# Optimization experiments

Hardware: AMD Instinct MI355X
Metric: run time of the kernel (lower is better)

The kernel has to match this reference:

```python
import jax, jax.numpy as jnp
from jax import lax
import numpy as np

B, N, G, K = 4, 1024, 128, 32
D_MODEL, DEPTH, CLS = 384, 12, 40
D_INNER, D_STATE, D_CONV, DT_RANK = 768, 16, 4, 24
EPS = 1e-5
BN_SCALE = 1.0 / float(np.sqrt(1.0 + EPS))  # eval BN, running_mean=0, running_var=1


def layernorm(x, w, b):
    mu = x.mean(-1, keepdims=True)
    var = ((x - mu) ** 2).mean(-1, keepdims=True)
    return (x - mu) * lax.rsqrt(var + EPS) * w + b


def bn_eval(x, g, b):
    return x * (g * BN_SCALE) + b


def fps(xyz, n):
    Bb, Nn, _ = xyz.shape
    first = jnp.zeros((Bb,), jnp.int32)

    def step(carry, _):
        dmin, last = carry
        p = jnp.take_along_axis(xyz, last[:, None, None], axis=1)  # B,1,3
        dmin = jnp.minimum(dmin, jnp.sum((xyz - p) ** 2, -1))
        nxt = jnp.argmax(dmin, -1).astype(jnp.int32)
        return (dmin, nxt), nxt

    _, rest = lax.scan(step, (jnp.full((Bb, Nn), 1e10, xyz.dtype), first), None, length=n - 1)
    return jnp.concatenate([first[None, :], rest], 0).T  # B,G


def group_points(xyz):
    idx = fps(xyz, G)
    center = jnp.take_along_axis(xyz, idx[:, :, None], axis=1)            # B,G,3
    d2 = jnp.sum((center[:, :, None, :] - xyz[:, None, :, :]) ** 2, -1)   # B,G,N
    _, knn = lax.top_k(-d2, K)                                            # B,G,K
    nb = jax.vmap(lambda p, i: p[i])(xyz, knn)                            # B,G,K,3
    return nb - center[:, :, None, :], center


def encoder(pg, w1, b1, g1, bb1, w2, b2, w3, b3, g2, bb2, w4, b4):
    Bb, Gg, Kk, _ = pg.shape
    f = pg.reshape(Bb * Gg, Kk, 3)
    f = jax.nn.relu(bn_eval(f @ w1.T + b1, g1, bb1))                      # BG,K,128
    f = f @ w2.T + b2                                                     # BG,K,256
    fg = f.max(1, keepdims=True)
    f = jnp.concatenate([jnp.broadcast_to(fg, f.shape), f], -1)           # BG,K,512
    f = jax.nn.relu(bn_eval(f @ w3.T + b3, g2, bb2))
    f = f @ w4.T + b4
    return f.max(1).reshape(Bb, Gg, -1)                                   # B,G,C


def mamba_mixer(x, ipw, cw, cb, xpw, dpw, dpb, A_log, Dp, opw):
    L = x.shape[1]
    xz = x @ ipw.T                                                        # B,L,2*Di
    u, z = jnp.split(xz, 2, -1)
    up = jnp.pad(u, ((0, 0), (D_CONV - 1, 0), (0, 0)))                    # causal depthwise conv
    u = sum(up[:, k:k + L, :] * cw[:, k] for k in range(D_CONV)) + cb
    u = jax.nn.silu(u)
    xdb = u @ xpw.T
    dt, Bm, Cm = jnp.split(xdb, [DT_RANK, DT_RANK + D_STATE], -1)
    dt = jax.nn.softplus(dt @ dpw.T + dpb)                                # B,L,Di
    A = -jnp.exp(A_log)                                                   # Di,Ds

    def step(h, inp):
        dt_t, B_t, C_t, u_t = inp
        h = jnp.exp(dt_t[:, :, None] * A) * h + (dt_t * u_t)[:, :, None] * B_t[:, None, :]
        return h, jnp.einsum('bds,bs->bd', h, C_t)

    h0 = jnp.zeros((x.shape[0], D_INNER, D_STATE), x.dtype)
    _, ys = lax.scan(step, h0, (dt.swapaxes(0, 1), Bm.swapaxes(0, 1), Cm.swapaxes(0, 1), u.swapaxes(0, 1)))
    y = ys.swapaxes(0, 1) + u * Dp
    return (y * jax.nn.silu(z)) @ opw.T


def forward(pts, enc_w1, enc_b1, enc_bn1_g, enc_bn1_b, enc_w2, enc_b2, enc_w3, enc_b3,
            enc_bn2_g, enc_bn2_b, enc_w4, enc_b4, pos_w1, pos_b1, pos_w2, pos_b2,
            ln_w, ln_b, in_proj_w, conv_w, conv_b, x_proj_w, dt_proj_w, dt_proj_b,
            A_log, D_param, out_proj_w, normf_w, normf_b, norm_w, norm_b,
            head_w1, head_b1, head_bn1_g, head_bn1_b, head_w2, head_b2,
            head_bn2_g, head_bn2_b, head_w3, head_b3):
    nb, center = group_points(pts)
    tok = encoder(nb, enc_w1, enc_b1, enc_bn1_g, enc_bn1_b, enc_w2, enc_b2,
                  enc_w3, enc_b3, enc_bn2_g, enc_bn2_b, enc_w4, enc_b4)    # B,G,384
    pos = jax.nn.gelu(center @ pos_w1.T + pos_b1, approximate=False) @ pos_w2.T + pos_b2

    # PointMamba token reordering: sort by center x, y, z and concatenate -> L = 3G
    toks, poss = [], []
    for ax in range(3):
        o = jnp.argsort(center[:, :, ax], axis=-1)[:, :, None]
        toks.append(jnp.take_along_axis(tok, o, axis=1))
        poss.append(jnp.take_along_axis(pos, o, axis=1))
    tok = jnp.concatenate(toks, 1)
    pos = jnp.concatenate(poss, 1)

    h = tok + pos
    res = jnp.zeros_like(h)

    def layer_step(carry, p):
        h, res = carry
        lnw, lnb, ipw, cw, cb, xpw, dpw, dpb, Al, Dp, opw = p
        res = h + res
        x = layernorm(res, lnw, lnb)
        h = mamba_mixer(x, ipw, cw, cb, xpw, dpw, dpb, Al, Dp, opw)
        return (h, res), None

    (h, res), _ = lax.scan(layer_step, (h, res),
                           (ln_w, ln_b, in_proj_w, conv_w, conv_b, x_proj_w,
                            dt_proj_w, dt_proj_b, A_log, D_param, out_proj_w))
    x = layernorm(h + res, normf_w, normf_b)   # MixerModel.norm_f
    x = layernorm(x, norm_w, norm_b)           # PointMamba.norm
    feat = x.mean(1)                           # B,384
    h1 = jax.nn.relu(bn_eval(feat @ head_w1.T + head_b1, head_bn1_g, head_bn1_b))
    h2 = jax.nn.relu(bn_eval(h1 @ head_w2.T + head_b2, head_bn2_g, head_bn2_b))
    return h2 @ head_w3.T + head_b3            # B,CLS


def setup_inputs():
    key = jax.random.key(0)
    ks = iter(jax.random.split(key, 64))

    def rn(shape, s=0.02):
        return jax.random.normal(next(ks), shape, jnp.float32) * s

    inp = dict(
        pts=jax.random.normal(next(ks), (B, N, 3), jnp.float32),
        enc_w1=rn((128, 3), 0.1), enc_b1=jnp.zeros((128,)),
        enc_bn1_g=jnp.ones((128,)), enc_bn1_b=jnp.zeros((128,)),
        enc_w2=rn((256, 128), 0.05), enc_b2=jnp.zeros((256,)),
        enc_w3=rn((512, 512), 0.05), enc_b3=jnp.zeros((512,)),
        enc_bn2_g=jnp.ones((512,)), enc_bn2_b=jnp.zeros((512,)),
        enc_w4=rn((D_MODEL, 512), 0.05), enc_b4=jnp.zeros((D_MODEL,)),
        pos_w1=rn((128, 3), 0.1), pos_b1=jnp.zeros((128,)),
        pos_w2=rn((D_MODEL, 128), 0.05), pos_b2=jnp.zeros((D_MODEL,)),
        ln_w=jnp.ones((DEPTH, D_MODEL)), ln_b=jnp.zeros((DEPTH, D_MODEL)),
        in_proj_w=rn((DEPTH, 2 * D_INNER, D_MODEL)),
        conv_w=rn((DEPTH, D_INNER, D_CONV), 0.2), conv_b=jnp.zeros((DEPTH, D_INNER)),
        x_proj_w=rn((DEPTH, DT_RANK + 2 * D_STATE, D_INNER)),
        dt_proj_w=rn((DEPTH, D_INNER, DT_RANK), 0.1),
        dt_proj_b=jnp.full((DEPTH, D_INNER), -4.6, jnp.float32),
        A_log=jnp.broadcast_to(jnp.log(jnp.arange(1, D_STATE + 1, dtype=jnp.float32)),
                               (DEPTH, D_INNER, D_STATE)).copy(),
        D_param=jnp.ones((DEPTH, D_INNER)),
        out_proj_w=rn((DEPTH, D_MODEL, D_INNER)),
        normf_w=jnp.ones((D_MODEL,)), normf_b=jnp.zeros((D_MODEL,)),
        norm_w=jnp.ones((D_MODEL,)), norm_b=jnp.zeros((D_MODEL,)),
        head_w1=rn((256, D_MODEL), 0.05), head_b1=jnp.zeros((256,)),
        head_bn1_g=jnp.ones((256,)), head_bn1_b=jnp.zeros((256,)),
        head_w2=rn((256, 256), 0.05), head_b2=jnp.zeros((256,)),
        head_bn2_g=jnp.ones((256,)), head_bn2_b=jnp.zeros((256,)),
        head_w3=rn((CLS, 256), 0.05), head_b3=jnp.zeros((CLS,)),
    )
    return inp


def reference(pts, enc_w1, enc_b1, enc_bn1_g, enc_bn1_b, enc_w2, enc_b2, enc_w3, enc_b3,
              enc_bn2_g, enc_bn2_b, enc_w4, enc_b4, pos_w1, pos_b1, pos_w2, pos_b2,
              ln_w, ln_b, in_proj_w, conv_w, conv_b, x_proj_w, dt_proj_w, dt_proj_b,
              A_log, D_param, out_proj_w, normf_w, normf_b, norm_w, norm_b,
              head_w1, head_b1, head_bn1_g, head_bn1_b, head_w2, head_b2,
              head_bn2_g, head_bn2_b, head_w3, head_b3):
    return forward(pts, enc_w1, enc_b1, enc_bn1_g, enc_bn1_b, enc_w2, enc_b2, enc_w3, enc_b3,
                   enc_bn2_g, enc_bn2_b, enc_w4, enc_b4, pos_w1, pos_b1, pos_w2, pos_b2,
                   ln_w, ln_b, in_proj_w, conv_w, conv_b, x_proj_w, dt_proj_w, dt_proj_b,
                   A_log, D_param, out_proj_w, normf_w, normf_b, norm_w, norm_b,
                   head_w1, head_b1, head_bn1_g, head_bn1_b, head_w2, head_b2,
                   head_bn2_g, head_bn2_b, head_w3, head_b3)
```

## Files before the change

kernel.cpp:

```cpp
#include <hip/hip_runtime.h>
#include <hip/hip_bf16.h>

using bf16 = __hip_bfloat16;
using short8  = __attribute__((ext_vector_type(8))) short;
using floatx4 = __attribute__((ext_vector_type(4))) float;
using ull = unsigned long long;

constexpr int Bn = 4, Np = 1024, Gn = 128, Kn = 32;
constexpr int DM = 384, DEPTH = 12, CLSn = 40;
constexpr int DI = 768, DSt = 16, DTR = 24;
constexpr int Ln = 384;
constexpr int NCH = 12, CHS = 32;
constexpr int NLC = 24;
constexpr float EPSf = 1e-5f;
constexpr float BNS = 0.99999500003749968752f;
constexpr float LOG2E = 1.4426950408889634f;

static __device__ __forceinline__ short f2bf(float f){
  bf16 h = __float2bfloat16(f);
  return *reinterpret_cast<short*>(&h);
}
static __device__ __forceinline__ float fsig(float x){ return 1.f/(1.f + __expf(-x)); }
static __device__ __forceinline__ float fsoftplus(float x){
  return fmaxf(x, 0.f) + __logf(1.f + __expf(-fabsf(x)));
}

template<int CTRL>
static __device__ __forceinline__ int dppmov(int x){
  return __builtin_amdgcn_update_dpp(0, x, CTRL, 0xF, 0xF, true);
}
static __device__ __forceinline__ ull redmax64(ull key){
  #define RSTEP(CTRL) { \
    int hi = (int)(unsigned)(key >> 32), lo = (int)(unsigned)key; \
    int h2 = dppmov<CTRL>(hi), l2 = dppmov<CTRL>(lo); \
    ull k2 = ((ull)(unsigned)h2 << 32) | (unsigned)l2; \
    if (k2 > key) key = k2; }
  RSTEP(0x111) RSTEP(0x112) RSTEP(0x114) RSTEP(0x118) RSTEP(0x142) RSTEP(0x143)
  #undef RSTEP
  return key;
}

__global__ __launch_bounds__(64) void fps_kernel(const float* __restrict__ pts,
                                                 float* __restrict__ center){
  int b = blockIdx.x, t = threadIdx.x;
  __shared__ float xs[1024], ys[1024], zs[1024];
  const float* p = pts + (size_t)b * Np * 3;
  float D[16];
  #pragma unroll
  for (int i = 0; i < 16; ++i){
    int n = t + 64*i;
    xs[n] = p[n*3+0]; ys[n] = p[n*3+1]; zs[n] = p[n*3+2];
    D[i] = 1e10f;
  }
  float px = xs[0], py = ys[0], pz = zs[0];
  if (t == 0){
    center[(size_t)(b*Gn)*3+0] = px;
    center[(size_t)(b*Gn)*3+1] = py;
    center[(size_t)(b*Gn)*3+2] = pz;
  }
  for (int it = 1; it < Gn; ++it){
    float v = -1.f; int nbest = t;
    #pragma unroll
    for (int i = 0; i < 16; ++i){
      int n = t + 64*i;
      float dx = __fsub_rn(xs[n], px);
      float dy = __fsub_rn(ys[n], py);
      float dz = __fsub_rn(zs[n], pz);
      float d  = __fadd_rn(__fadd_rn(__fmul_rn(dx,dx), __fmul_rn(dy,dy)), __fmul_rn(dz,dz));
      float dm = fminf(D[i], d); D[i] = dm;
      if (dm > v){ v = dm; nbest = n; }
    }
    ull key = ((ull)__float_as_uint(v) << 32) | (unsigned)(Np-1 - nbest);
    key = redmax64(key);
    int lo63 = __builtin_amdgcn_readlane((int)(unsigned)(key & 0xFFFFFFFFu), 63);
    int wn = Np-1 - lo63;
    wn = min(max(wn, 0), Np-1);
    px = xs[wn]; py = ys[wn]; pz = zs[wn];
    if (t == 0){
      center[(size_t)(b*Gn+it)*3+0] = px;
      center[(size_t)(b*Gn+it)*3+1] = py;
      center[(size_t)(b*Gn+it)*3+2] = pz;
    }
  }
}

__global__ __launch_bounds__(256) void knn_kernel(const float* __restrict__ pts,
                                                  const float* __restrict__ center,
                                                  float* __restrict__ nb){
  int gid = blockIdx.x; int b = gid >> 7;
  __shared__ float d2[1024];
  __shared__ float rv[4]; __shared__ int ri[4];
  int t = threadIdx.x;
  float cx = center[(size_t)gid*3+0], cy = center[(size_t)gid*3+1], cz = center[(size_t)gid*3+2];
  const float* p = pts + (size_t)b * Np * 3;
  for (int n = t; n < Np; n += 256){
    float dx = __fsub_rn(cx, p[n*3+0]);
    float dy = __fsub_rn(cy, p[n*3+1]);
    float dz = __fsub_rn(cz, p[n*3+2]);
    d2[n] = __fadd_rn(__fadd_rn(__fmul_rn(dx,dx), __fmul_rn(dy,dy)), __fmul_rn(dz,dz));
  }
  __syncthreads();
  for (int kk = 0; kk < Kn; ++kk){
    float v = 3e38f; int idx = 0;
    for (int n = t; n < Np; n += 256){
      float d = d2[n];
      if (d < v || (d == v && n < idx)){ v = d; idx = n; }
    }
    ull key = ((ull)(unsigned)(~__float_as_uint(v)) << 32) | (unsigned)(Np-1 - idx);
    key = redmax64(key);
    if ((t & 63) == 63){
      rv[t>>6] = __uint_as_float(~(unsigned)(key >> 32));
      ri[t>>6] = Np-1 - (int)(unsigned)(key & 0xFFFFFFFFu);
    }
    __syncthreads();
    if (t == 0){
      float bv = rv[0]; int bi = ri[0];
      for (int w = 1; w < 4; ++w){
        if (rv[w] < bv || (rv[w] == bv && ri[w] < bi)){ bv = rv[w]; bi = ri[w]; }
      }
      bi = min(max(bi, 0), Np-1);
      nb[((size_t)gid*Kn+kk)*3+0] = __fsub_rn(p[bi*3+0], cx);
      nb[((size_t)gid*Kn+kk)*3+1] = __fsub_rn(p[bi*3+1], cy);
      nb[((size_t)gid*Kn+kk)*3+2] = __fsub_rn(p[bi*3+2], cz);
      d2[bi] = 3e38f;
    }
    __syncthreads();
  }
}

__global__ __launch_bounds__(256) void cvt_bf16(const float* __restrict__ s,
                                                bf16* __restrict__ d, int n){
  int i = (blockIdx.x*256 + threadIdx.x)*4;
  if (i < n){
    float4 v = *(const float4*)(s + i);
    short* o = (short*)d + i;
    o[0] = f2bf(v.x); o[1] = f2bf(v.y); o[2] = f2bf(v.z); o[3] = f2bf(v.w);
  }
}

template<typename AT, typename WT, int ACT, int GATE>
__global__ __launch_bounds__(256) void gemm_mfma(const AT* __restrict__ A, int lda,
                                                 const WT* __restrict__ W,
                                                 const float* __restrict__ bias,
                                                 const float* __restrict__ g,
                                                 const float* __restrict__ bb,
                                                 float* __restrict__ C, int ldc,
                                                 int M, int N, int K){
  __shared__ __align__(16) short As[64*40];
  __shared__ __align__(16) short Ws[64*40];
  int bm = blockIdx.x * 64, bn = blockIdx.y * 64;
  int t = threadIdx.x;
  int row = t >> 2;
  int kseg = (t & 3) * 8;
  int w = t >> 6, lane = t & 63, m16 = lane & 15, q = lane >> 4;
  bool kvec = ((K & 3) == 0) && ((lda & 3) == 0 || sizeof(AT) == 2);
  floatx4 acc[4] = {};
  for (int k0 = 0; k0 < K; k0 += 32){
    if constexpr (GATE){
      const float* Ar = (const float*)A + (size_t)(bm + row)*lda + k0 + kseg;
      float4 y0 = *(const float4*)Ar;
      float4 y1 = *(const float4*)(Ar + 4);
      float4 z0 = *(const float4*)(Ar + 768);
      float4 z1 = *(const float4*)(Ar + 772);
      short* dst = &As[row*40 + kseg];
      dst[0] = f2bf(y0.x * (z0.x * fsig(z0.x)));
      dst[1] = f2bf(y0.y * (z0.y * fsig(z0.y)));
      dst[2] = f2bf(y0.z * (z0.z * fsig(z0.z)));
      dst[3] = f2bf(y0.w * (z0.w * fsig(z0.w)));
      dst[4] = f2bf(y1.x * (z1.x * fsig(z1.x)));
      dst[5] = f2bf(y1.y * (z1.y * fsig(z1.y)));
      dst[6] = f2bf(y1.z * (z1.z * fsig(z1.z)));
      dst[7] = f2bf(y1.w * (z1.w * fsig(z1.w)));
    } else if constexpr (sizeof(AT) == 2){
      *(short8*)&As[row*40 + kseg] =
          *(const short8*)((const short*)A + (size_t)(bm + row)*lda + k0 + kseg);
    } else {
      const float* Ar = (const float*)A + (size_t)(bm + row)*lda;
      short* dst = &As[row*40 + kseg];
      if (kvec && (k0 + kseg + 8 <= K)){
        float4 a0 = *(const float4*)(Ar + k0 + kseg);
        float4 a1 = *(const float4*)(Ar + k0 + kseg + 4);
        dst[0]=f2bf(a0.x); dst[1]=f2bf(a0.y); dst[2]=f2bf(a0.z); dst[3]=f2bf(a0.w);
        dst[4]=f2bf(a1.x); dst[5]=f2bf(a1.y); dst[6]=f2bf(a1.z); dst[7]=f2bf(a1.w);
      } else {
        #pragma unroll
        for (int j = 0; j < 8; ++j){
          int k = k0 + kseg + j;
          dst[j] = (k < K) ? f2bf(Ar[k]) : (short)0;
        }
      }
    }
    if constexpr (sizeof(WT) == 2){
      int n = bn + row;
      short8 v;
      #pragma unroll
      for (int j = 0; j < 8; ++j) v[j] = 0;
      if (n < N) v = *(const short8*)((const short*)W + (size_t)n*K + k0 + kseg);
      *(short8*)&Ws[row*40 + kseg] = v;
    } else {
      int n = bn + row;
      short* dst = &Ws[row*40 + kseg];
      if (n < N && ((K & 3) == 0) && (k0 + kseg + 8 <= K)){
        const float* Wr = (const float*)W + (size_t)n*K + k0 + kseg;
        float4 w0 = *(const float4*)Wr;
        float4 w1 = *(const float4*)(Wr + 4);
        dst[0]=f2bf(w0.x); dst[1]=f2bf(w0.y); dst[2]=f2bf(w0.z); dst[3]=f2bf(w0.w);
        dst[4]=f2bf(w1.x); dst[5]=f2bf(w1.y); dst[6]=f2bf(w1.z); dst[7]=f2bf(w1.w);
      } else {
        #pragma unroll
        for (int j = 0; j < 8; ++j){
          int k = k0 + kseg + j;
          dst[j] = (n < N && k < K) ? f2bf(((const float*)W)[(size_t)n*K + k]) : (short)0;
        }
      }
    }
    __syncthreads();
    short8 af = *(const short8*)&As[(w*16 + m16)*40 + q*8];
    #pragma unroll
    for (int j = 0; j < 4; ++j){
      short8 bfr = *(const short8*)&Ws[(j*16 + m16)*40 + q*8];
      acc[j] = __builtin_amdgcn_mfma_f32_16x16x32_bf16(af, bfr, acc[j], 0, 0, 0);
    }
    __syncthreads();
  }
  #pragma unroll
  for (int j = 0; j < 4; ++j){
    int n = bn + j*16 + m16;
    if (n < N){
      float bv = bias ? bias[n] : 0.f;
      float gv = 0.f, bbv = 0.f;
      if (ACT == 1){ gv = g[n] * BNS; bbv = bb[n]; }
      #pragma unroll
      for (int r = 0; r < 4; ++r){
        int m = bm + w*16 + q*4 + r;
        float v = acc[j][r] + bv;
        if (ACT == 1){ v = v * gv + bbv; v = fmaxf(v, 0.f); }
        C[(size_t)m*ldc + n] = v;
      }
    }
  }
}

__global__ __launch_bounds__(256) void maxk_fg(float* __restrict__ f3in){
  int gg = blockIdx.x; int c = threadIdx.x;
  float m = -3e38f;
  for (int k = 0; k < Kn; ++k) m = fmaxf(m, f3in[((size_t)gg*Kn + k)*512 + 256 + c]);
  for (int k = 0; k < Kn; ++k) f3in[((size_t)gg*Kn + k)*512 + c] = m;
}

__global__ __launch_bounds__(384) void maxk_tok(const float* __restrict__ f4, float* __restrict__ tok){
  int gg = blockIdx.x; int c = threadIdx.x;
  float m = -3e38f;
  for (int k = 0; k < Kn; ++k) m = fmaxf(m, f4[((size_t)gg*Kn + k)*DM + c]);
  tok[(size_t)gg*DM + c] = m;
}

__global__ __launch_bounds__(128) void pos_kernel(const float* __restrict__ center,
                                                  const float* __restrict__ w1, const float* __restrict__ b1,
                                                  const float* __restrict__ w2, const float* __restrict__ b2,
                                                  float* __restrict__ tok){
  int gid = blockIdx.x;
  __shared__ float h1[128]; __shared__ float c3[3];
  int t = threadIdx.x;
  if (t < 3) c3[t] = center[(size_t)gid*3 + t];
  __syncthreads();
  float a = w1[t*3+0]*c3[0] + w1[t*3+1]*c3[1] + w1[t*3+2]*c3[2] + b1[t];
  h1[t] = 0.5f * a * (1.f + erff(a * 0.70710678118654752440f));
  __syncthreads();
  for (int c = t; c < DM; c += 128){
    float s = b2[c];
    for (int j = 0; j < 128; ++j) s += w2[(size_t)c*128 + j] * h1[j];
    tok[(size_t)gid*DM + c] += s;
  }
}

__global__ __launch_bounds__(128) void sort_kernel(const float* __restrict__ center,
                                                   int* __restrict__ order){
  int bax = blockIdx.x; int b = bax / 3, ax = bax % 3;
  __shared__ float key[128];
  int t = threadIdx.x;
  key[t] = center[(size_t)(b*Gn + t)*3 + ax];
  __syncthreads();
  float kt = key[t]; int r = 0;
  for (int j = 0; j < Gn; ++j){
    float kj = key[j];
    r += (kj < kt || (kj == kt && j < t)) ? 1 : 0;
  }
  r = min(max(r, 0), Gn-1);
  order[b*Ln + ax*Gn + r] = t;
}

__global__ __launch_bounds__(256) void build_h(const float* __restrict__ tok,
                        const int* __restrict__ order,
                        float* __restrict__ h, float* __restrict__ res){
  int i = blockIdx.x * blockDim.x + threadIdx.x;
  if (i >= Bn*Ln*DM) return;
  int c = i % DM; int l = (i / DM) % Ln; int b = i / (DM*Ln);
  int src = order[b*Ln + l];
  src = min(max(src, 0), Gn-1);
  h[i] = tok[((size_t)(b*Gn + src))*DM + c];
  res[i] = 0.f;
}

__global__ __launch_bounds__(256) void ln_res_kernel(const float* __restrict__ h,
                                                     float* __restrict__ res,
                                                     bf16* __restrict__ x,
                                                     const float* __restrict__ w,
                                                     const float* __restrict__ bias){
  int wv = threadIdx.x >> 6, ln = threadIdx.x & 63;
  int tokid = blockIdx.x*4 + wv;
  const float* hr = h + (size_t)tokid*DM;
  float* rr = res + (size_t)tokid*DM;
  bf16* xr = x + (size_t)tokid*DM;
  float v[6]; float s = 0.f;
  #pragma unroll
  for (int i = 0; i < 6; ++i){ int c = ln + 64*i; float t = hr[c] + rr[c]; rr[c] = t; v[i] = t; s += t; }
  #pragma unroll
  for (int o = 32; o > 0; o >>= 1) s += __shfl_xor(s, o);
  float mu = s * (1.f/DM);
  float q = 0.f;
  #pragma unroll
  for (int i = 0; i < 6; ++i){ float d = v[i] - mu; q += d*d; }
  #pragma unroll
  for (int o = 32; o > 0; o >>= 1) q += __shfl_xor(q, o);
  float rstd = rsqrtf(q * (1.f/DM) + EPSf);
  #pragma unroll
  for (int i = 0; i < 6; ++i){ int c = ln + 64*i;
    xr[c] = __float2bfloat16((v[i]-mu)*rstd*w[c] + bias[c]); }
}

__global__ __launch_bounds__(256) void conv_fused(const float* __restrict__ xz,
                                                  float* __restrict__ ucv,
                                                  const float* __restrict__ cw,
                                                  const float* __restrict__ cb){
  int blk = blockIdx.x;
  int lc = blk % NLC; int bd = blk / NLC; int dch = bd % 3; int b = bd / 3;
  int t = threadIdx.x; int d = dch*256 + t;
  int l0 = lc*16;
  float w0 = cw[d*4+0], w1 = cw[d*4+1], w2 = cw[d*4+2], w3 = cw[d*4+3];
  float bias = cb[d];
  float u0 = (l0 >= 3) ? xz[((size_t)(b*Ln + l0-3))*1536 + d] : 0.f;
  float u1 = (l0 >= 2) ? xz[((size_t)(b*Ln + l0-2))*1536 + d] : 0.f;
  float u2 = (l0 >= 1) ? xz[((size_t)(b*Ln + l0-1))*1536 + d] : 0.f;
  const float* pin = xz + ((size_t)(b*Ln + l0))*1536 + d;
  float* pout = ucv + ((size_t)(b*Ln + l0))*DI + d;
  float r[16];
  #pragma unroll
  for (int i = 0; i < 16; ++i) r[i] = pin[(size_t)i*1536];
  #pragma unroll
  for (int i = 0; i < 16; ++i){
    float v = u0*w0 + u1*w1 + u2*w2 + r[i]*w3 + bias;
    pout[(size_t)i*DI] = v * fsig(v);
    u0 = u1; u1 = u2; u2 = r[i];
  }
}

__global__ __launch_bounds__(256) void conv_save(const float* __restrict__ xz,
                                                 float* __restrict__ bnd){
  int blk = blockIdx.x;
  int lc = blk % NLC; int bd = blk / NLC; int dch = bd % 3; int b = bd / 3;
  int t = threadIdx.x; int d = dch*256 + t;
  int l0 = lc*16;
  #pragma unroll
  for (int j = 0; j < 3; ++j){
    int l = l0 - 3 + j;
    float v = (l >= 0) ? xz[((size_t)(b*Ln + l))*1536 + d] : 0.f;
    bnd[(((size_t)blk)*3 + j)*256 + t] = v;
  }
}

__global__ __launch_bounds__(256) void conv_apply(float* __restrict__ xz,
                                                  const float* __restrict__ bnd,
                                                  const float* __restrict__ cw,
                                                  const float* __restrict__ cb){
  int blk = blockIdx.x;
  int lc = blk % NLC; int bd = blk / NLC; int dch = bd % 3; int b = bd / 3;
  int t = threadIdx.x; int d = dch*256 + t;
  int l0 = lc*16;
  float w0 = cw[d*4+0], w1 = cw[d*4+1], w2 = cw[d*4+2], w3 = cw[d*4+3];
  float bias = cb[d];
  float u0 = bnd[(((size_t)blk)*3 + 0)*256 + t];
  float u1 = bnd[(((size_t)blk)*3 + 1)*256 + t];
  float u2 = bnd[(((size_t)blk)*3 + 2)*256 + t];
  float* p = xz + ((size_t)(b*Ln + l0))*1536 + d;
  float r[16];
  #pragma unroll
  for (int i = 0; i < 16; ++i) r[i] = p[(size_t)i*1536];
  #pragma unroll
  for (int i = 0; i < 16; ++i){
    float v = u0*w0 + u1*w1 + u2*w2 + r[i]*w3 + bias;
    p[(size_t)i*1536] = v * fsig(v);
    u0 = u1; u1 = u2; u2 = r[i];
  }
}

__global__ __launch_bounds__(256) void scanA_kernel(const float* __restrict__ usrc, int uld,
                                                    const float* __restrict__ xdb,
                                                    const float* __restrict__ dpw,
                                                    const float* __restrict__ dpb,
                                                    const float* __restrict__ A_log,
                                                    float* __restrict__ SB_S,
                                                    float* __restrict__ SB_dt){
  __shared__ float sRow[CHS*56];
  __shared__ float sU[CHS*256];
  int blk = blockIdx.x;
  int c = blk % NCH; int bd = blk / NCH; int dch = bd % 3; int b = bd / 3;
  int t = threadIdx.x; int d = dch*256 + t;
  int l0 = c*CHS;
  for (int i = t; i < CHS*56; i += 256) sRow[i] = xdb[((size_t)(b*Ln + l0))*56 + i];
  const float* up = usrc + ((size_t)(b*Ln + l0))*uld + dch*256;
  #pragma unroll
  for (int i = 0; i < CHS; ++i) sU[i*256 + t] = up[(size_t)i*uld + t];
  float w[DTR];
  const float* wp = dpw + (size_t)d*DTR;
  #pragma unroll
  for (int j = 0; j < DTR; ++j) w[j] = wp[j];
  float a2[DSt], h[DSt];
  const float* ap = A_log + (size_t)d*DSt;
  #pragma unroll
  for (int s = 0; s < DSt; ++s){ a2[s] = -__expf(ap[s]) * LOG2E; h[s] = 0.f; }
  float dbias = dpb[d];
  float sumdt = 0.f;
  __syncthreads();
  for (int i = 0; i < CHS; ++i){
    int ro = i*56;
    float dtr = dbias;
    #pragma unroll
    for (int j = 0; j < DTR; ++j) dtr += w[j] * sRow[ro + j];
    float dtv = fsoftplus(dtr);
    sumdt += dtv;
    float du = dtv * sU[i*256 + t];
    #pragma unroll
    for (int s = 0; s < DSt; ++s)
      h[s] = exp2f(dtv * a2[s]) * h[s] + du * sRow[ro + 24 + s];
  }
  size_t sb = ((size_t)blk*256 + t)*16;
  #pragma unroll
  for (int s = 0; s < DSt; ++s) SB_S[sb + s] = h[s];
  SB_dt[(size_t)blk*256 + t] = sumdt;
}

__global__ __launch_bounds__(256) void scanB_kernel(float* __restrict__ xz,
                                                    const float* __restrict__ usrc, int uld,
                                                    const float* __restrict__ xdb,
                                                    const float* __restrict__ dpw,
                                                    const float* __restrict__ dpb,
                                                    const float* __restrict__ A_log,
                                                    const float* __restrict__ Dp,
                                                    const float* __restrict__ SB_S,
                                                    const float* __restrict__ SB_dt){
  __shared__ float sRow[CHS*56];
  __shared__ float sU[CHS*256];
  int blk = blockIdx.x;
  int c = blk % NCH; int bd = blk / NCH; int dch = bd % 3; int b = bd / 3;
  int t = threadIdx.x; int d = dch*256 + t;
  int l0 = c*CHS;
  for (int i = t; i < CHS*56; i += 256) sRow[i] = xdb[((size_t)(b*Ln + l0))*56 + i];
  const float* up = usrc + ((size_t)(b*Ln + l0))*uld + dch*256;
  #pragma unroll
  for (int i = 0; i < CHS; ++i) sU[i*256 + t] = up[(size_t)i*uld + t];
  float w[DTR];
  const float* wp = dpw + (size_t)d*DTR;
  #pragma unroll
  for (int j = 0; j < DTR; ++j) w[j] = wp[j];
  float a2[DSt], h[DSt];
  const float* ap = A_log + (size_t)d*DSt;
  #pragma unroll
  for (int s = 0; s < DSt; ++s){ a2[s] = -__expf(ap[s]) * LOG2E; h[s] = 0.f; }
  for (int cc = 0; cc < c; ++cc){
    size_t base = (((size_t)bd*NCH + cc)*256 + t)*16;
    float sd = SB_dt[((size_t)bd*NCH + cc)*256 + t];
    #pragma unroll
    for (int s = 0; s < DSt; ++s)
      h[s] = exp2f(sd * a2[s]) * h[s] + SB_S[base + s];
  }
  float dbias = dpb[d];
  float Dd = Dp[d];
  float* ydst = xz + ((size_t)(b*Ln + l0))*1536 + dch*256;
  __syncthreads();
  for (int i = 0; i < CHS; ++i){
    int ro = i*56;
    float dtr = dbias;
    #pragma unroll
    for (int j = 0; j < DTR; ++j) dtr += w[j] * sRow[ro + j];
    float dtv = fsoftplus(dtr);
    float u = sU[i*256 + t];
    float du = dtv * u;
    float yv = 0.f;
    #pragma unroll
    for (int s = 0; s < DSt; ++s){
      h[s] = exp2f(dtv * a2[s]) * h[s] + du * sRow[ro + 24 + s];
      yv += h[s] * sRow[ro + 40 + s];
    }
    ydst[(size_t)i*1536 + t] = yv + u*Dd;
  }
}

__global__ __launch_bounds__(256) void final_ln_kernel(const float* __restrict__ h,
                                                       const float* __restrict__ res,
                                                       const float* w1, const float* b1,
                                                       const float* w2, const float* b2,
                                                       float* __restrict__ x){
  int wv = threadIdx.x >> 6, ln = threadIdx.x & 63;
  int tokid = blockIdx.x*4 + wv;
  const float* hr = h + (size_t)tokid*DM;
  const float* rr = res + (size_t)tokid*DM;
  float* xr = x + (size_t)tokid*DM;
  float v[6]; float s = 0.f;
  #pragma unroll
  for (int i = 0; i < 6; ++i){ int c = ln + 64*i; v[i] = hr[c] + rr[c]; s += v[i]; }
  #pragma unroll
  for (int o = 32; o > 0; o >>= 1) s += __shfl_xor(s, o);
  float mu = s * (1.f/DM); float q = 0.f;
  #pragma unroll
  for (int i = 0; i < 6; ++i){ float dd = v[i]-mu; q += dd*dd; }
  #pragma unroll
  for (int o = 32; o > 0; o >>= 1) q += __shfl_xor(q, o);
  float rstd = rsqrtf(q * (1.f/DM) + EPSf);
  float u[6]; float s2 = 0.f;
  #pragma unroll
  for (int i = 0; i < 6; ++i){ int c = ln + 64*i; u[i] = (v[i]-mu)*rstd*w1[c] + b1[c]; s2 += u[i]; }
  #pragma unroll
  for (int o = 32; o > 0; o >>= 1) s2 += __shfl_xor(s2, o);
  float mu2 = s2 * (1.f/DM); float q2 = 0.f;
  #pragma unroll
  for (int i = 0; i < 6; ++i){ float dd = u[i]-mu2; q2 += dd*dd; }
  #pragma unroll
  for (int o = 32; o > 0; o >>= 1) q2 += __shfl_xor(q2, o);
  float rstd2 = rsqrtf(q2 * (1.f/DM) + EPSf);
  #pragma unroll
  for (int i = 0; i < 6; ++i){ int c = ln + 64*i; xr[c] = (u[i]-mu2)*rstd2*w2[c] + b2[c]; }
}

__global__ __launch_bounds__(384) void head_kernel(const float* __restrict__ x,
    const float* w1, const float* b1, const float* g1, const float* bb1,
    const float* w2, const float* b2, const float* g2, const float* bb2,
    const float* w3, const float* b3, float* __restrict__ out){
  int b = blockIdx.x; int t = threadIdx.x;
  __shared__ float feat[DM]; __shared__ float h1[256]; __shared__ float h2[256];
  float s = 0.f;
  for (int l = 0; l < Ln; ++l) s += x[((size_t)(b*Ln + l))*DM + t];
  feat[t] = s * (1.f/Ln);
  __syncthreads();
  if (t < 256){
    float a = b1[t];
    for (int j = 0; j < DM; ++j) a += w1[(size_t)t*DM + j] * feat[j];
    a = a * (g1[t] * BNS) + bb1[t];
    h1[t] = fmaxf(a, 0.f);
  }
  __syncthreads();
  if (t < 256){
    float a = b2[t];
    for (int j = 0; j < 256; ++j) a += w2[(size_t)t*256 + j] * h1[j];
    a = a * (g2[t] * BNS) + bb2[t];
    h2[t] = fmaxf(a, 0.f);
  }
  __syncthreads();
  if (t < CLSn){
    float a = b3[t];
    for (int j = 0; j < 256; ++j) a += w3[(size_t)t*256 + j] * h2[j];
    out[b*CLSn + t] = a;
  }
}

extern "C" void kernel_launch(void* const* d_in, const int* in_sizes, int n_in,
                              void* d_out, int out_size, void* d_ws, size_t ws_size,
                              hipStream_t stream) {
  if (n_in < 42) return;
  if (out_size < Bn*CLSn) return;
  constexpr size_t WS_FLOATS = 3919936;
  if (ws_size < WS_FLOATS * sizeof(float)) return;
  constexpr size_t MIDF = 5812224;
  constexpr size_t BIGF = 18874368;
  const bool mid = ws_size >= (WS_FLOATS + MIDF) * sizeof(float);
  const bool big = ws_size >= (WS_FLOATS + MIDF + BIGF) * sizeof(float);

  const float* pts       = (const float*)d_in[0];
  const float* enc_w1    = (const float*)d_in[1];  const float* enc_b1    = (const float*)d_in[2];
  const float* enc_bn1_g = (const float*)d_in[3];  const float* enc_bn1_b = (const float*)d_in[4];
  const float* enc_w2    = (const float*)d_in[5];  const float* enc_b2    = (const float*)d_in[6];
  const float* enc_w3    = (const float*)d_in[7];  const float* enc_b3    = (const float*)d_in[8];
  const float* enc_bn2_g = (const float*)d_in[9];  const float* enc_bn2_b = (const float*)d_in[10];
  const float* enc_w4    = (const float*)d_in[11]; const float* enc_b4    = (const float*)d_in[12];
  const float* pos_w1    = (const float*)d_in[13]; const float* pos_b1    = (const float*)d_in[14];
  const float* pos_w2    = (const float*)d_in[15]; const float* pos_b2    = (const float*)d_in[16];
  const float* ln_w      = (const float*)d_in[17]; const float* ln_b      = (const float*)d_in[18];
  const float* in_proj_w = (const float*)d_in[19];
  const float* conv_w    = (const float*)d_in[20]; const float* conv_b    = (const float*)d_in[21];
  const float* x_proj_w  = (const float*)d_in[22];
  const float* dt_proj_w = (const float*)d_in[23]; const float* dt_proj_b = (const float*)d_in[24];
  const float* A_log     = (const float*)d_in[25]; const float* D_param   = (const float*)d_in[26];
  const float* out_proj_w= (const float*)d_in[27];
  const float* normf_w   = (const float*)d_in[28]; const float* normf_b   = (const float*)d_in[29];
  const float* norm_w    = (const float*)d_in[30]; const float* norm_b    = (const float*)d_in[31];
  const float* head_w1   = (const float*)d_in[32]; const float* head_b1   = (const float*)d_in[33];
  const float* head_bn1_g= (const float*)d_in[34]; const float* head_bn1_b= (const float*)d_in[35];
  const float* head_w2   = (const float*)d_in[36]; const float* head_b2   = (const float*)d_in[37];
  const float* head_bn2_g= (const float*)d_in[38]; const float* head_bn2_b= (const float*)d_in[39];
  const float* head_w3   = (const float*)d_in[40]; const float* head_b3   = (const float*)d_in[41];

  float* ws = (float*)d_ws;
  float* hb   = ws;
  float* resb = ws + 589824;
  float* U    = ws + 1179648;
  float* center = U;
  float* nb     = U + 1536;
  float* tok    = U + 50688;
  int*   order  = (int*)(U + 247296);
  float* eb0    = U + 262144;
  float* eb1    = U + 1310720;
  float* xz   = U;
  float* xdb  = U + 2359296;
  bf16*  xb   = (bf16*)(U + 2445312);
  float* SBdt = U + 2445312;
  float* BND  = U + 2482176;
  float* SBS  = hb;
  float* xf   = U;
  float* WB = ws + WS_FLOATS;
  bf16* wb_ip = (bf16*)WB;
  bf16* wb_op = (bf16*)(WB + 3538944);
  bf16* wb_xp = (bf16*)(WB + 5308416);
  bf16* wb_e2 = (bf16*)(WB + 5566464);
  bf16* wb_e3 = (bf16*)(WB + 5582848);
  bf16* wb_e4 = (bf16*)(WB + 5713920);
  float* F3in = WB + MIDF;
  float* F3   = WB + MIDF + 8388608;
  float* F1   = WB + MIDF + 16777216;
  float* F4   = F3in;
  float* ucv  = F3in;

  if (mid){
    cvt_bf16<<<(12*1536*384/4 + 255)/256, 256, 0, stream>>>(in_proj_w, wb_ip, 12*1536*384);
    cvt_bf16<<<(12*384*768/4 + 255)/256, 256, 0, stream>>>(out_proj_w, wb_op, 12*384*768);
    cvt_bf16<<<(12*56*768/4 + 255)/256, 256, 0, stream>>>(x_proj_w, wb_xp, 12*56*768);
    cvt_bf16<<<(256*128/4 + 255)/256, 256, 0, stream>>>(enc_w2, wb_e2, 256*128);
    cvt_bf16<<<(512*512/4 + 255)/256, 256, 0, stream>>>(enc_w3, wb_e3, 512*512);
    cvt_bf16<<<(384*512/4 + 255)/256, 256, 0, stream>>>(enc_w4, wb_e4, 384*512);
  }

  fps_kernel<<<Bn, 64, 0, stream>>>(pts, center);
  knn_kernel<<<Bn*Gn, 256, 0, stream>>>(pts, center, nb);

  if (big){
    gemm_mfma<float,float,1,0><<<dim3(256,2), 256, 0, stream>>>(nb, 3, enc_w1, enc_b1,
        enc_bn1_g, enc_bn1_b, F1, 128, 16384, 128, 3);
    gemm_mfma<float,bf16,0,0><<<dim3(256,4), 256, 0, stream>>>(F1, 128, wb_e2, enc_b2,
        nullptr, nullptr, F3in + 256, 512, 16384, 256, 128);
    maxk_fg<<<512, 256, 0, stream>>>(F3in);
    gemm_mfma<float,bf16,1,0><<<dim3(256,8), 256, 0, stream>>>(F3in, 512, wb_e3, enc_b3,
        enc_bn2_g, enc_bn2_b, F3, 512, 16384, 512, 512);
    gemm_mfma<float,bf16,0,0><<<dim3(256,6), 256, 0, stream>>>(F3, 512, wb_e4, enc_b4,
        nullptr, nullptr, F4, 384, 16384, 384, 512);
    maxk_tok<<<512, 384, 0, stream>>>(F4, tok);
  } else {
    for (int ch = 0; ch < 8; ++ch){
      const float* nb_c = nb + (size_t)ch*2048*3;
      float* tok_c = tok + (size_t)ch*64*DM;
      gemm_mfma<float,float,1,0><<<dim3(32,2), 256, 0, stream>>>(nb_c, 3, enc_w1, enc_b1,
          enc_bn1_g, enc_bn1_b, eb1, 128, 2048, 128, 3);
      if (mid){
        gemm_mfma<float,bf16,0,0><<<dim3(32,4), 256, 0, stream>>>(eb1, 128, wb_e2, enc_b2,
            nullptr, nullptr, eb0 + 256, 512, 2048, 256, 128);
        maxk_fg<<<64, 256, 0, stream>>>(eb0);
        gemm_mfma<float,bf16,1,0><<<dim3(32,8), 256, 0, stream>>>(eb0, 512, wb_e3, enc_b3,
            enc_bn2_g, enc_bn2_b, eb1, 512, 2048, 512, 512);
        gemm_mfma<float,bf16,0,0><<<dim3(32,6), 256, 0, stream>>>(eb1, 512, wb_e4, enc_b4,
            nullptr, nullptr, eb0, 384, 2048, 384, 512);
      } else {
        gemm_mfma<float,float,0,0><<<dim3(32,4), 256, 0, stream>>>(eb1, 128, enc_w2, enc_b2,
            nullptr, nullptr, eb0 + 256, 512, 2048, 256, 128);
        maxk_fg<<<64, 256, 0, stream>>>(eb0);
        gemm_mfma<float,float,1,0><<<dim3(32,8), 256, 0, stream>>>(eb0, 512, enc_w3, enc_b3,
            enc_bn2_g, enc_bn2_b, eb1, 512, 2048, 512, 512);
        gemm_mfma<float,float,0,0><<<dim3(32,6), 256, 0, stream>>>(eb1, 512, enc_w4, enc_b4,
            nullptr, nullptr, eb0, 384, 2048, 384, 512);
      }
      maxk_tok<<<64, 384, 0, stream>>>(eb0, tok_c);
    }
  }

  pos_kernel<<<Bn*Gn, 128, 0, stream>>>(center, pos_w1, pos_b1, pos_w2, pos_b2, tok);
  sort_kernel<<<Bn*3, 128, 0, stream>>>(center, order);
  build_h<<<(Bn*Ln*DM + 255)/256, 256, 0, stream>>>(tok, order, hb, resb);

  for (int l = 0; l < DEPTH; ++l){
    const float* lnw  = ln_w      + (size_t)l*DM;
    const float* lnb  = ln_b      + (size_t)l*DM;
    const float* ipw  = in_proj_w + (size_t)l*1536*DM;
    const float* cw   = conv_w    + (size_t)l*DI*4;
    const float* cb   = conv_b    + (size_t)l*DI;
    const float* xpw  = x_proj_w  + (size_t)l*56*DI;
    const float* dpw  = dt_proj_w + (size_t)l*DI*DTR;
    const float* dpb  = dt_proj_b + (size_t)l*DI;
    const float* Alg  = A_log     + (size_t)l*DI*DSt;
    const float* Dpar = D_param   + (size_t)l*DI;
    const float* opw  = out_proj_w+ (size_t)l*DM*DI;

    ln_res_kernel<<<Bn*Ln/4, 256, 0, stream>>>(hb, resb, xb, lnw, lnb);
    if (mid){
      gemm_mfma<bf16,bf16,0,0><<<dim3(24,24), 256, 0, stream>>>(xb, DM,
          wb_ip + (size_t)l*1536*DM, nullptr, nullptr, nullptr, xz, 1536, Bn*Ln, 1536, DM);
    } else {
      gemm_mfma<bf16,float,0,0><<<dim3(24,24), 256, 0, stream>>>(xb, DM, ipw,
          nullptr, nullptr, nullptr, xz, 1536, Bn*Ln, 1536, DM);
    }
    if (big){
      conv_fused<<<Bn*3*NLC, 256, 0, stream>>>(xz, ucv, cw, cb);
      if (mid)
        gemm_mfma<float,bf16,0,0><<<dim3(24,1), 256, 0, stream>>>(ucv, DI,
            wb_xp + (size_t)l*56*DI, nullptr, nullptr, nullptr, xdb, 56, Bn*Ln, 56, DI);
      else
        gemm_mfma<float,float,0,0><<<dim3(24,1), 256, 0, stream>>>(ucv, DI, xpw,
            nullptr, nullptr, nullptr, xdb, 56, Bn*Ln, 56, DI);
      scanA_kernel<<<Bn*3*NCH, 256, 0, stream>>>(ucv, DI, xdb, dpw, dpb, Alg, SBS, SBdt);
      scanB_kernel<<<Bn*3*NCH, 256, 0, stream>>>(xz, ucv, DI, xdb, dpw, dpb, Alg, Dpar, SBS, SBdt);
    } else {
      conv_save<<<Bn*3*NLC, 256, 0, stream>>>(xz, BND);
      conv_apply<<<Bn*3*NLC, 256, 0, stream>>>(xz, BND, cw, cb);
      if (mid)
        gemm_mfma<float,bf16,0,0><<<dim3(24,1), 256, 0, stream>>>(xz, 1536,
            wb_xp + (size_t)l*56*DI, nullptr, nullptr, nullptr, xdb, 56, Bn*Ln, 56, DI);
      else
        gemm_mfma<float,float,0,0><<<dim3(24,1), 256, 0, stream>>>(xz, 1536, xpw,
            nullptr, nullptr, nullptr, xdb, 56, Bn*Ln, 56, DI);
      scanA_kernel<<<Bn*3*NCH, 256, 0, stream>>>(xz, 1536, xdb, dpw, dpb, Alg, SBS, SBdt);
      scanB_kernel<<<Bn*3*NCH, 256, 0, stream>>>(xz, xz, 1536, xdb, dpw, dpb, Alg, Dpar, SBS, SBdt);
    }
    if (mid){
      gemm_mfma<float,bf16,0,1><<<dim3(24,6), 256, 0, stream>>>(xz, 1536,
          wb_op + (size_t)l*DM*DI, nullptr, nullptr, nullptr, hb, DM, Bn*Ln, DM, DI);
    } else {
      gemm_mfma<float,float,0,1><<<dim3(24,6), 256, 0, stream>>>(xz, 1536, opw,
          nullptr, nullptr, nullptr, hb, DM, Bn*Ln, DM, DI);
    }
  }

  final_ln_kernel<<<Bn*Ln/4, 256, 0, stream>>>(hb, resb, normf_w, normf_b, norm_w, norm_b, xf);
  head_kernel<<<Bn, 384, 0, stream>>>(xf, head_w1, head_b1, head_bn1_g, head_bn1_b,
                                      head_w2, head_b2, head_bn2_g, head_bn2_b,
                                      head_w3, head_b3, (float*)d_out);
}
```

Baseline: 1.786 ms.

## Fuse causal conv into x_proj GEMM and scan kernels, halve scan chunk size

Removes the separate conv_fused kernel on the big-workspace path. The depthwise causal conv plus SiLU is recomputed inside the x_proj GEMM's A-tile load and inside both scan kernels. The scan now writes y to a separate buffer with 16-row chunks, doubling the number of blocks. The gated out_proj GEMM reads y and z from different buffers. FPS keeps point coordinates in registers instead of re-reading LDS, and adds a missing sync; the trade-off is redundant conv arithmetic and extra xz reads, in exchange for fewer launches and a lost intermediate write.

New measurement: 2.074 ms. +16.2%, slower.

```diff
diff --git a/kernel.cpp b/kernel.cpp
--- a/kernel.cpp
+++ b/kernel.cpp
@@ -10,7 +10,6 @@
 constexpr int DM = 384, DEPTH = 12, CLSn = 40;
 constexpr int DI = 768, DSt = 16, DTR = 24;
 constexpr int Ln = 384;
-constexpr int NCH = 12, CHS = 32;
 constexpr int NLC = 24;
 constexpr float EPSf = 1e-5f;
 constexpr float BNS = 0.99999500003749968752f;
@@ -45,13 +44,16 @@
   int b = blockIdx.x, t = threadIdx.x;
   __shared__ float xs[1024], ys[1024], zs[1024];
   const float* p = pts + (size_t)b * Np * 3;
-  float D[16];
+  float X[16], Y[16], Z[16], D[16];
   #pragma unroll
   for (int i = 0; i < 16; ++i){
     int n = t + 64*i;
-    xs[n] = p[n*3+0]; ys[n] = p[n*3+1]; zs[n] = p[n*3+2];
+    float a = p[n*3+0], c = p[n*3+1], e = p[n*3+2];
+    X[i] = a; Y[i] = c; Z[i] = e;
+    xs[n] = a; ys[n] = c; zs[n] = e;
     D[i] = 1e10f;
   }
+  __syncthreads();
   float px = xs[0], py = ys[0], pz = zs[0];
   if (t == 0){
     center[(size_t)(b*Gn)*3+0] = px;
@@ -62,13 +64,12 @@
     float v = -1.f; int nbest = t;
     #pragma unroll
     for (int i = 0; i < 16; ++i){
-      int n = t + 64*i;
-      float dx = __fsub_rn(xs[n], px);
-      float dy = __fsub_rn(ys[n], py);
-      float dz = __fsub_rn(zs[n], pz);
+      float dx = __fsub_rn(X[i], px);
+      float dy = __fsub_rn(Y[i], py);
+      float dz = __fsub_rn(Z[i], pz);
       float d  = __fadd_rn(__fadd_rn(__fmul_rn(dx,dx), __fmul_rn(dy,dy)), __fmul_rn(dz,dz));
       float dm = fminf(D[i], d); D[i] = dm;
-      if (dm > v){ v = dm; nbest = n; }
+      if (dm > v){ v = dm; nbest = t + 64*i; }
     }
     ull key = ((ull)__float_as_uint(v) << 32) | (unsigned)(Np-1 - nbest);
     key = redmax64(key);
@@ -138,12 +139,12 @@
   }
 }
 
-template<typename AT, typename WT, int ACT, int GATE>
+template<typename AT, typename WT, int ACT, int MODE>
 __global__ __launch_bounds__(256) void gemm_mfma(const AT* __restrict__ A, int lda,
                                                  const WT* __restrict__ W,
                                                  const float* __restrict__ bias,
-                                                 const float* __restrict__ g,
-                                                 const float* __restrict__ bb,
+                                                 const float* __restrict__ gz,
+                                                 const float* __restrict__ bbp,
                                                  float* __restrict__ C, int ldc,
                                                  int M, int N, int K){
   __shared__ __align__(16) short As[64*40];
@@ -156,21 +157,36 @@
   bool kvec = ((K & 3) == 0) && ((lda & 3) == 0 || sizeof(AT) == 2);
   floatx4 acc[4] = {};
   for (int k0 = 0; k0 < K; k0 += 32){
-    if constexpr (GATE){
-      const float* Ar = (const float*)A + (size_t)(bm + row)*lda + k0 + kseg;
-      float4 y0 = *(const float4*)Ar;
-      float4 y1 = *(const float4*)(Ar + 4);
-      float4 z0 = *(const float4*)(Ar + 768);
-      float4 z1 = *(const float4*)(Ar + 772);
+    if constexpr (MODE == 1){
+      const float* Yr = (const float*)A + (size_t)(bm + row)*lda + k0 + kseg;
+      const float* Zr = gz + (size_t)(bm + row)*1536 + 768 + k0 + kseg;
+      float y[8], z[8];
+      *(float4*)&y[0] = *(const float4*)Yr;  *(float4*)&y[4] = *(const float4*)(Yr + 4);
+      *(float4*)&z[0] = *(const float4*)Zr;  *(float4*)&z[4] = *(const float4*)(Zr + 4);
       short* dst = &As[row*40 + kseg];
-      dst[0] = f2bf(y0.x * (z0.x * fsig(z0.x)));
-      dst[1] = f2bf(y0.y * (z0.y * fsig(z0.y)));
-      dst[2] = f2bf(y0.z * (z0.z * fsig(z0.z)));
-      dst[3] = f2bf(y0.w * (z0.w * fsig(z0.w)));
-      dst[4] = f2bf(y1.x * (z1.x * fsig(z1.x)));
-      dst[5] = f2bf(y1.y * (z1.y * fsig(z1.y)));
-      dst[6] = f2bf(y1.z * (z1.z * fsig(z1.z)));
-      dst[7] = f2bf(y1.w * (z1.w * fsig(z1.w)));
+      #pragma unroll
+      for (int jj = 0; jj < 8; ++jj) dst[jj] = f2bf(y[jj] * (z[jj] * fsig(z[jj])));
+    } else if constexpr (MODE == 2){
+      int m = bm + row;
+      int bq = m / Ln, lq = m - bq*Ln;
+      const float* Xb = (const float*)A + ((size_t)bq*Ln)*1536 + k0 + kseg;
+      float r0[8] = {}, r1[8] = {}, r2[8] = {}, r3[8];
+      *(float4*)&r3[0] = *(const float4*)(Xb + (size_t)lq*1536);
+      *(float4*)&r3[4] = *(const float4*)(Xb + (size_t)lq*1536 + 4);
+      if (lq >= 1){ *(float4*)&r2[0] = *(const float4*)(Xb + (size_t)(lq-1)*1536);
+                    *(float4*)&r2[4] = *(const float4*)(Xb + (size_t)(lq-1)*1536 + 4); }
+      if (lq >= 2){ *(float4*)&r1[0] = *(const float4*)(Xb + (size_t)(lq-2)*1536);
+                    *(float4*)&r1[4] = *(const float4*)(Xb + (size_t)(lq-2)*1536 + 4); }
+      if (lq >= 3){ *(float4*)&r0[0] = *(const float4*)(Xb + (size_t)(lq-3)*1536);
+                    *(float4*)&r0[4] = *(const float4*)(Xb + (size_t)(lq-3)*1536 + 4); }
+      short* dst = &As[row*40 + kseg];
+      #pragma unroll
+      for (int jj = 0; jj < 8; ++jj){
+        int dcol = k0 + kseg + jj;
+        float u = gz[dcol*4+0]*r0[jj] + gz[dcol*4+1]*r1[jj]
+                + gz[dcol*4+2]*r2[jj] + gz[dcol*4+3]*r3[jj] + bbp[dcol];
+        dst[jj] = f2bf(u * fsig(u));
+      }
     } else if constexpr (sizeof(AT) == 2){
       *(short8*)&As[row*40 + kseg] =
           *(const short8*)((const short*)A + (size_t)(bm + row)*lda + k0 + kseg);
@@ -229,7 +245,7 @@
     if (n < N){
       float bv = bias ? bias[n] : 0.f;
       float gv = 0.f, bbv = 0.f;
-      if (ACT == 1){ gv = g[n] * BNS; bbv = bb[n]; }
+      if (ACT == 1){ gv = gz[n] * BNS; bbv = bbp[n]; }
       #pragma unroll
       for (int r = 0; r < 4; ++r){
         int m = bm + w*16 + q*4 + r;
@@ -327,32 +343,6 @@
   #pragma unroll
   for (int i = 0; i < 6; ++i){ int c = ln + 64*i;
     xr[c] = __float2bfloat16((v[i]-mu)*rstd*w[c] + bias[c]); }
-}
-
-__global__ __launch_bounds__(256) void conv_fused(const float* __restrict__ xz,
-                                                  float* __restrict__ ucv,
-                                                  const float* __restrict__ cw,
-                                                  const float* __restrict__ cb){
-  int blk = blockIdx.x;
-  int lc = blk % NLC; int bd = blk / NLC; int dch = bd % 3; int b = bd / 3;
-  int t = threadIdx.x; int d = dch*256 + t;
-  int l0 = lc*16;
-  float w0 = cw[d*4+0], w1 = cw[d*4+1], w2 = cw[d*4+2], w3 = cw[d*4+3];
-  float bias = cb[d];
-  float u0 = (l0 >= 3) ? xz[((size_t)(b*Ln + l0-3))*1536 + d] : 0.f;
-  float u1 = (l0 >= 2) ? xz[((size_t)(b*Ln + l0-2))*1536 + d] : 0.f;
-  float u2 = (l0 >= 1) ? xz[((size_t)(b*Ln + l0-1))*1536 + d] : 0.f;
-  const float* pin = xz + ((size_t)(b*Ln + l0))*1536 + d;
-  float* pout = ucv + ((size_t)(b*Ln + l0))*DI + d;
-  float r[16];
-  #pragma unroll
-  for (int i = 0; i < 16; ++i) r[i] = pin[(size_t)i*1536];
-  #pragma unroll
-  for (int i = 0; i < 16; ++i){
-    float v = u0*w0 + u1*w1 + u2*w2 + r[i]*w3 + bias;
-    pout[(size_t)i*DI] = v * fsig(v);
-    u0 = u1; u1 = u2; u2 = r[i];
-  }
 }
 
 __global__ __launch_bounds__(256) void conv_save(const float* __restrict__ xz,
@@ -394,23 +384,43 @@
   }
 }
 
-__global__ __launch_bounds__(256) void scanA_kernel(const float* __restrict__ usrc, int uld,
+template<int CHSt>
+__global__ __launch_bounds__(256) void scanA_kernel(const float* __restrict__ xz_u, int uld, int convf,
+                                                    const float* __restrict__ cw,
+                                                    const float* __restrict__ cb,
                                                     const float* __restrict__ xdb,
                                                     const float* __restrict__ dpw,
                                                     const float* __restrict__ dpb,
                                                     const float* __restrict__ A_log,
                                                     float* __restrict__ SB_S,
                                                     float* __restrict__ SB_dt){
-  __shared__ float sRow[CHS*56];
-  __shared__ float sU[CHS*256];
+  constexpr int NCHt = Ln / CHSt;
+  __shared__ float sRow[CHSt*56];
+  __shared__ float sU[CHSt*256];
   int blk = blockIdx.x;
-  int c = blk % NCH; int bd = blk / NCH; int dch = bd % 3; int b = bd / 3;
+  int c = blk % NCHt; int bd = blk / NCHt; int dch = bd % 3; int b = bd / 3;
   int t = threadIdx.x; int d = dch*256 + t;
-  int l0 = c*CHS;
-  for (int i = t; i < CHS*56; i += 256) sRow[i] = xdb[((size_t)(b*Ln + l0))*56 + i];
-  const float* up = usrc + ((size_t)(b*Ln + l0))*uld + dch*256;
-  #pragma unroll
-  for (int i = 0; i < CHS; ++i) sU[i*256 + t] = up[(size_t)i*uld + t];
+  int l0 = c*CHSt;
+  for (int i = t; i < CHSt*56; i += 256) sRow[i] = xdb[((size_t)(b*Ln + l0))*56 + i];
+  if (convf){
+    const float* X = xz_u + ((size_t)b*Ln)*1536 + d;
+    float w0 = cw[d*4+0], w1 = cw[d*4+1], w2 = cw[d*4+2], w3 = cw[d*4+3];
+    float cbv = cb[d];
+    float u0 = (l0 >= 3) ? X[(size_t)(l0-3)*1536] : 0.f;
+    float u1 = (l0 >= 2) ? X[(size_t)(l0-2)*1536] : 0.f;
+    float u2 = (l0 >= 1) ? X[(size_t)(l0-1)*1536] : 0.f;
+    #pragma unroll
+    for (int i = 0; i < CHSt; ++i){
+      float xv = X[(size_t)(l0+i)*1536];
+      float v = u0*w0 + u1*w1 + u2*w2 + xv*w3 + cbv;
+      sU[i*256 + t] = v * fsig(v);
+      u0 = u1; u1 = u2; u2 = xv;
+    }
+  } else {
+    const float* up = xz_u + ((size_t)(b*Ln + l0))*uld + dch*256;
+    #pragma unroll
+    for (int i = 0; i < CHSt; ++i) sU[i*256 + t] = up[(size_t)i*uld + t];
+  }
   float w[DTR];
   const float* wp = dpw + (size_t)d*DTR;
   #pragma unroll
@@ -422,7 +432,7 @@
   float dbias = dpb[d];
   float sumdt = 0.f;
   __syncthreads();
-  for (int i = 0; i < CHS; ++i){
+  for (int i = 0; i < CHSt; ++i){
     int ro = i*56;
     float dtr = dbias;
     #pragma unroll
@@ -440,8 +450,11 @@
   SB_dt[(size_t)blk*256 + t] = sumdt;
 }
 
-__global__ __launch_bounds__(256) void scanB_kernel(float* __restrict__ xz,
-                                                    const float* __restrict__ usrc, int uld,
+template<int CHSt>
+__global__ __launch_bounds__(256) void scanB_kernel(float* __restrict__ ydst_base, int ys,
+                                                    const float* __restrict__ xz_u, int uld, int convf,
+                                                    const float* __restrict__ cw,
+                                                    const float* __restrict__ cb,
                                                     const float* __restrict__ xdb,
                                                     const float* __restrict__ dpw,
                                                     const float* __restrict__ dpb,
@@ -449,16 +462,33 @@
                                                     const float* __restrict__ Dp,
                                                     const float* __restrict__ SB_S,
                                                     const float* __restrict__ SB_dt){
-  __shared__ float sRow[CHS*56];
-  __shared__ float sU[CHS*256];
+  constexpr int NCHt = Ln / CHSt;
+  __shared__ float sRow[CHSt*56];
+  __shared__ float sU[CHSt*256];
   int blk = blockIdx.x;
-  int c = blk % NCH; int bd = blk / NCH; int dch = bd % 3; int b = bd / 3;
+  int c = blk % NCHt; int bd = blk / NCHt; int dch = bd % 3; int b = bd / 3;
   int t = threadIdx.x; int d = dch*256 + t;
-  int l0 = c*CHS;
-  for (int i = t; i < CHS*56; i += 256) sRow[i] = xdb[((size_t)(b*Ln + l0))*56 + i];
-  const float* up = usrc + ((size_t)(b*Ln + l0))*uld + dch*256;
-  #pragma unroll
-  for (int i = 0; i < CHS; ++i) sU[i*256 + t] = up[(size_t)i*uld + t];
+  int l0 = c*CHSt;
+  for (int i = t; i < CHSt*56; i += 256) sRow[i] = xdb[((size_t)(b*Ln + l0))*56 + i];
+  if (convf){
+    const float* X = xz_u + ((size_t)b*Ln)*1536 + d;
+    float w0 = cw[d*4+0], w1 = cw[d*4+1], w2 = cw[d*4+2], w3 = cw[d*4+3];
+    float cbv = cb[d];
+    float u0 = (l0 >= 3) ? X[(size_t)(l0-3)*1536] : 0.f;
+    float u1 = (l0 >= 2) ? X[(size_t)(l0-2)*1536] : 0.f;
+    float u2 = (l0 >= 1) ? X[(size_t)(l0-1)*1536] : 0.f;
+    #pragma unroll
+    for (int i = 0; i < CHSt; ++i){
+      float xv = X[(size_t)(l0+i)*1536];
+      float v = u0*w0 + u1*w1 + u2*w2 + xv*w3 + cbv;
+      sU[i*256 + t] = v * fsig(v);
+      u0 = u1; u1 = u2; u2 = xv;
+    }
+  } else {
+    const float* up = xz_u + ((size_t)(b*Ln + l0))*uld + dch*256;
+    #pragma unroll
+    for (int i = 0; i < CHSt; ++i) sU[i*256 + t] = up[(size_t)i*uld + t];
+  }
   float w[DTR];
   const float* wp = dpw + (size_t)d*DTR;
   #pragma unroll
@@ -468,17 +498,17 @@
   #pragma unroll
   for (int s = 0; s < DSt; ++s){ a2[s] = -__expf(ap[s]) * LOG2E; h[s] = 0.f; }
   for (int cc = 0; cc < c; ++cc){
-    size_t base = (((size_t)bd*NCH + cc)*256 + t)*16;
-    float sd = SB_dt[((size_t)bd*NCH + cc)*256 + t];
+    size_t base = (((size_t)bd*NCHt + cc)*256 + t)*16;
+    float sd = SB_dt[((size_t)bd*NCHt + cc)*256 + t];
     #pragma unroll
     for (int s = 0; s < DSt; ++s)
       h[s] = exp2f(sd * a2[s]) * h[s] + SB_S[base + s];
   }
   float dbias = dpb[d];
   float Dd = Dp[d];
-  float* ydst = xz + ((size_t)(b*Ln + l0))*1536 + dch*256;
-  __syncthreads();
-  for (int i = 0; i < CHS; ++i){
+  float* ydst = ydst_base + ((size_t)(b*Ln + l0))*ys + dch*256;
+  __syncthreads();
+  for (int i = 0; i < CHSt; ++i){
     int ro = i*56;
     float dtr = dbias;
     #pragma unroll
@@ -492,7 +522,7 @@
       h[s] = exp2f(dtv * a2[s]) * h[s] + du * sRow[ro + 24 + s];
       yv += h[s] * sRow[ro + 40 + s];
     }
-    ydst[(size_t)i*1536 + t] = yv + u*Dd;
+    ydst[(size_t)i*ys + t] = yv + u*Dd;
   }
 }
 
@@ -612,9 +642,9 @@
   float* xz   = U;
   float* xdb  = U + 2359296;
   bf16*  xb   = (bf16*)(U + 2445312);
-  float* SBdt = U + 2445312;
+  float* SBdt_s = U + 2445312;
   float* BND  = U + 2482176;
-  float* SBS  = hb;
+  float* SBS_s  = hb;
   float* xf   = U;
   float* WB = ws + WS_FLOATS;
   bf16* wb_ip = (bf16*)WB;
@@ -628,6 +658,8 @@
   float* F1   = WB + MIDF + 16777216;
   float* F4   = F3in;
   float* ucv  = F3in;
+  float* SBS_b  = F3;
+  float* SBdt_b = F1;
 
   if (mid){
     cvt_bf16<<<(12*1536*384/4 + 255)/256, 256, 0, stream>>>(in_proj_w, wb_ip, 12*1536*384);
@@ -705,15 +737,22 @@
           nullptr, nullptr, nullptr, xz, 1536, Bn*Ln, 1536, DM);
     }
     if (big){
-      conv_fused<<<Bn*3*NLC, 256, 0, stream>>>(xz, ucv, cw, cb);
       if (mid)
-        gemm_mfma<float,bf16,0,0><<<dim3(24,1), 256, 0, stream>>>(ucv, DI,
-            wb_xp + (size_t)l*56*DI, nullptr, nullptr, nullptr, xdb, 56, Bn*Ln, 56, DI);
+        gemm_mfma<float,bf16,0,2><<<dim3(24,1), 256, 0, stream>>>(xz, 1536,
+            wb_xp + (size_t)l*56*DI, nullptr, cw, cb, xdb, 56, Bn*Ln, 56, DI);
       else
-        gemm_mfma<float,float,0,0><<<dim3(24,1), 256, 0, stream>>>(ucv, DI, xpw,
-            nullptr, nullptr, nullptr, xdb, 56, Bn*Ln, 56, DI);
-      scanA_kernel<<<Bn*3*NCH, 256, 0, stream>>>(ucv, DI, xdb, dpw, dpb, Alg, SBS, SBdt);
-      scanB_kernel<<<Bn*3*NCH, 256, 0, stream>>>(xz, ucv, DI, xdb, dpw, dpb, Alg, Dpar, SBS, SBdt);
+        gemm_mfma<float,float,0,2><<<dim3(24,1), 256, 0, stream>>>(xz, 1536, xpw,
+            nullptr, cw, cb, xdb, 56, Bn*Ln, 56, DI);
+      scanA_kernel<16><<<Bn*3*(Ln/16), 256, 0, stream>>>(xz, 1536, 1, cw, cb,
+          xdb, dpw, dpb, Alg, SBS_b, SBdt_b);
+      scanB_kernel<16><<<Bn*3*(Ln/16), 256, 0, stream>>>(ucv, DI, xz, 1536, 1, cw, cb,
+          xdb, dpw, dpb, Alg, Dpar, SBS_b, SBdt_b);
+      if (mid)
+        gemm_mfma<float,bf16,0,1><<<dim3(24,6), 256, 0, stream>>>(ucv, DI,
+            wb_op + (size_t)l*DM*DI, nullptr, xz, nullptr, hb, DM, Bn*Ln, DM, DI);
+      else
+        gemm_mfma<float,float,0,1><<<dim3(24,6), 256, 0, stream>>>(ucv, DI, opw,
+            nullptr, xz, nullptr, hb, DM, Bn*Ln, DM, DI);
     } else {
       conv_save<<<Bn*3*NLC, 256, 0, stream>>>(xz, BND);
       conv_apply<<<Bn*3*NLC, 256, 0, stream>>>(xz, BND, cw, cb);
@@ -723,15 +762,16 @@
       else
         gemm_mfma<float,float,0,0><<<dim3(24,1), 256, 0, stream>>>(xz, 1536, xpw,
             nullptr, nullptr, nullptr, xdb, 56, Bn*Ln, 56, DI);
-      scanA_kernel<<<Bn*3*NCH, 256, 0, stream>>>(xz, 1536, xdb, dpw, dpb, Alg, SBS, SBdt);
-      scanB_kernel<<<Bn*3*NCH, 256, 0, stream>>>(xz, xz, 1536, xdb, dpw, dpb, Alg, Dpar, SBS, SBdt);
-    }
-    if (mid){
-      gemm_mfma<float,bf16,0,1><<<dim3(24,6), 256, 0, stream>>>(xz, 1536,
-          wb_op + (size_t)l*DM*DI, nullptr, nullptr, nullptr, hb, DM, Bn*Ln, DM, DI);
-    } else {
-      gemm_mfma<float,float,0,1><<<dim3(24,6), 256, 0, stream>>>(xz, 1536, opw,
-          nullptr, nullptr, nullptr, hb, DM, Bn*Ln, DM, DI);
+      scanA_kernel<32><<<Bn*3*(Ln/32), 256, 0, stream>>>(xz, 1536, 0, nullptr, nullptr,
+          xdb, dpw, dpb, Alg, SBS_s, SBdt_s);
+      scanB_kernel<32><<<Bn*3*(Ln/32), 256, 0, stream>>>(xz, 1536, xz, 1536, 0, nullptr, nullptr,
+          xdb, dpw, dpb, Alg, Dpar, SBS_s, SBdt_s);
+      if (mid)
+        gemm_mfma<float,bf16,0,1><<<dim3(24,6), 256, 0, stream>>>(xz, 1536,
+            wb_op + (size_t)l*DM*DI, nullptr, xz, nullptr, hb, DM, Bn*Ln, DM, DI);
+      else
+        gemm_mfma<float,float,0,1><<<dim3(24,6), 256, 0, stream>>>(xz, 1536, opw,
+            nullptr, xz, nullptr, hb, DM, Bn*Ln, DM, DI);
     }
   }
 
```
